# Optimization experiments

Measured on AMD Instinct MI355X. Metric: run time of the kernel, lower is better.

The kernel has to match this reference:

```python
import jax, jax.numpy as jnp
import numpy as np


def setup_inputs() -> dict:
    key = jax.random.key(0)
    k1, k2, k3 = jax.random.split(key, 3)
    B, Q, K, D = 4, 2048, 2048, 1024
    query = jax.random.normal(k1, (B, Q, D), dtype=jnp.float32)
    value = jax.random.normal(k2, (B, K, D), dtype=jnp.float32)
    attention_mask = jax.random.randint(k3, (B, Q, K), 0, 2, dtype=jnp.int32)
    return {"query": query, "value": value, "attention_mask": attention_mask}


def reference(query, value, attention_mask):
    # key defaults to value in the original module
    D = query.shape[-1]
    # scores[b,q,k] = sum_d (query[b,q,d] + key[b,k,d])
    #              = rowsum(query)[b,q] + rowsum(key)[b,k]  (separable outer-sum,
    # avoids the (B,Q,K,D) intermediate the torch code materializes)
    q_sum = query.sum(-1)                    # (B, Q)
    k_sum = value.sum(-1)                    # (B, K)  (key == value)
    scores = q_sum[:, :, None] + k_sum[:, None, :]   # (B, Q, K)
    scores = scores / jnp.sqrt(jnp.asarray(D, scores.dtype))  # use_scale=True
    mask_value = -1e9
    scores = scores + (1.0 - attention_mask.astype(scores.dtype)) * mask_value
    attention_weights = jax.nn.softmax(scores, axis=-1)       # (B, Q, K)
    context_vector = jnp.einsum('bqk,bkd->bqd', attention_weights, value)
    return (context_vector, attention_weights)
```

## Files before the change

kernel.cpp:

```cpp
#include <hip/hip_runtime.h>
#include <stdint.h>

#define BB 4
#define QQ 2048
#define KK 2048
#define DD 1024

__device__ inline unsigned short f2bf(float f) {
    unsigned int u = __float_as_uint(f);
    unsigned int r = (u + 0x7fffu + ((u >> 16) & 1u)) >> 16;
    return (unsigned short)r;
}

typedef short bf16x8 __attribute__((ext_vector_type(8)));
typedef float f32x4  __attribute__((ext_vector_type(4)));

__device__ inline void async16(const void* g, void* l) {
    __builtin_amdgcn_global_load_lds(
        (const __attribute__((address_space(1))) unsigned int*)g,
        (__attribute__((address_space(3))) unsigned int*)l,
        16, 0, 0);
}

__global__ __launch_bounds__(256) void transpose_sum(const float* __restrict__ V,
                                                     unsigned short* __restrict__ Vt,
                                                     float* __restrict__ s) {
    int bid = blockIdx.x;
    int b  = bid >> 9;
    int r  = bid & 511;
    int kt = r >> 4;
    int dt = r & 15;
    int k0 = kt * 64, d0 = dt * 64;
    __shared__ float tile[64 * 65];
    int t = threadIdx.x;
    for (int i = 0; i < 4; i++) {
        int idx = i * 256 + t;
        int row = idx >> 4;
        int c4  = idx & 15;
        float4 v = *(const float4*)(V + (size_t)(b * KK + k0 + row) * DD + d0 + c4 * 4);
        float* p = &tile[row * 65 + c4 * 4];
        p[0] = v.x; p[1] = v.y; p[2] = v.z; p[3] = v.w;
        float ps = (v.x + v.y) + (v.z + v.w);
        ps += __shfl_xor(ps, 8, 16);
        ps += __shfl_xor(ps, 4, 16);
        ps += __shfl_xor(ps, 2, 16);
        ps += __shfl_xor(ps, 1, 16);
        if (c4 == 0) atomicAdd(s + (size_t)b * KK + k0 + row, ps);
    }
    __syncthreads();
    for (int i = 0; i < 4; i++) {
        int idx = i * 256 + t;
        int dr = idx >> 4;
        int kc = idx & 15;
        ushort4 o;
        o.x = f2bf(tile[(kc * 4 + 0) * 65 + dr]);
        o.y = f2bf(tile[(kc * 4 + 1) * 65 + dr]);
        o.z = f2bf(tile[(kc * 4 + 2) * 65 + dr]);
        o.w = f2bf(tile[(kc * 4 + 3) * 65 + dr]);
        *(ushort4*)(Vt + (size_t)(b * DD + d0 + dr) * KK + k0 + kc * 4) = o;
    }
}

__global__ __launch_bounds__(256) void weights_k(const int* __restrict__ mask,
                                                 const float* __restrict__ s,
                                                 float* __restrict__ wout,
                                                 unsigned short* __restrict__ wb16) {
    int wave = threadIdx.x >> 6, lane = threadIdx.x & 63;
    int row = blockIdx.x * 4 + wave;
    int b = row >> 11;
    const int4*   mp = (const int4*)(mask + (size_t)row * KK);
    const float4* ep = (const float4*)(s + (size_t)b * KK);
    float4 w[8];
    float ss = 0.f;
    for (int j = 0; j < 8; j++) {
        int4   m  = mp[lane + j * 64];
        float4 sv = ep[lane + j * 64];
        float4 ev;
        ev.x = __expf(sv.x * 0.03125f);
        ev.y = __expf(sv.y * 0.03125f);
        ev.z = __expf(sv.z * 0.03125f);
        ev.w = __expf(sv.w * 0.03125f);
        w[j].x = m.x ? ev.x : 0.f;
        w[j].y = m.y ? ev.y : 0.f;
        w[j].z = m.z ? ev.z : 0.f;
        w[j].w = m.w ? ev.w : 0.f;
        ss += (w[j].x + w[j].y) + (w[j].z + w[j].w);
    }
    for (int off = 32; off; off >>= 1) ss += __shfl_xor(ss, off, 64);
    float rS = 1.f / ss;
    float4*  wp = (float4*)(wout + (size_t)row * KK);
    ushort4* bp = (ushort4*)(wb16 + (size_t)row * KK);
    for (int j = 0; j < 8; j++) {
        float4 v = w[j];
        v.x *= rS; v.y *= rS; v.z *= rS; v.w *= rS;
        wp[lane + j * 64] = v;
        ushort4 pk;
        pk.x = f2bf(v.x); pk.y = f2bf(v.y); pk.z = f2bf(v.z); pk.w = f2bf(v.w);
        bp[lane + j * 64] = pk;
    }
}

__global__ __launch_bounds__(256) void gemm_ctx(const unsigned short* __restrict__ Wb,
                                                const unsigned short* __restrict__ Vt,
                                                float* __restrict__ ctx) {
    int bid = blockIdx.x;
    int dt = bid >> 6;
    int b  = (bid >> 4) & 3;
    int qt = bid & 15;
    int q0 = qt * 128, n0 = dt * 128;
    __shared__ unsigned short As[2][128 * 64];
    __shared__ unsigned short Bs[2][128 * 64];
    int tid = threadIdx.x, wave = tid >> 6, lane = tid & 63;
    int quad = lane >> 4, lm = lane & 15;
    int wm = wave >> 1, wn = wave & 1;

    int srow   = lane >> 3;
    int schunk = (lane & 7) ^ srow;
    const unsigned short* Ag = Wb + (size_t)(b * QQ + q0 + wave * 8 + srow) * KK + schunk * 8;
    const unsigned short* Bg = Vt + (size_t)(b * DD + n0 + wave * 8 + srow) * KK + schunk * 8;
    unsigned short* lA0 = &As[0][(wave * 8) * 64];
    unsigned short* lA1 = &As[1][(wave * 8) * 64];
    unsigned short* lB0 = &Bs[0][(wave * 8) * 64];
    unsigned short* lB1 = &Bs[1][(wave * 8) * 64];

    int m7 = lm & 7;
    int xa0 = lm * 64 + ((0 + quad) ^ m7) * 8;
    int xa1 = lm * 64 + ((4 + quad) ^ m7) * 8;

    f32x4 acc[4][4];
    for (int i = 0; i < 4; i++)
        for (int j = 0; j < 4; j++) acc[i][j] = 0.f;

#define STAGE(dA, dB, kpos) do {                                           \
        for (int c = 0; c < 4; c++) {                                      \
            async16(Ag + (size_t)(c * 32) * KK + (kpos), (dA) + c * 32 * 64); \
            async16(Bg + (size_t)(c * 32) * KK + (kpos), (dB) + c * 32 * 64); \
        }                                                                  \
    } while (0)

#define COMPUTE(Ab, Bb) do {                                               \
        bf16x8 a[4][2], bv[4][2];                                          \
        for (int i = 0; i < 4; i++) {                                      \
            a[i][0]  = *(const bf16x8*)&(Ab)[(wm * 64 + i * 16) * 64 + xa0]; \
            a[i][1]  = *(const bf16x8*)&(Ab)[(wm * 64 + i * 16) * 64 + xa1]; \
            bv[i][0] = *(const bf16x8*)&(Bb)[(wn * 64 + i * 16) * 64 + xa0]; \
            bv[i][1] = *(const bf16x8*)&(Bb)[(wn * 64 + i * 16) * 64 + xa1]; \
        }                                                                  \
        for (int h = 0; h < 2; h++)                                        \
            for (int i = 0; i < 4; i++)                                    \
                for (int j = 0; j < 4; j++)                                \
                    acc[i][j] = __builtin_amdgcn_mfma_f32_16x16x32_bf16(   \
                        a[i][h], bv[j][h], acc[i][j], 0, 0, 0);            \
    } while (0)

#define DRAIN_BARRIER() do {                                               \
        __builtin_amdgcn_sched_barrier(0);                                 \
        asm volatile("s_waitcnt vmcnt(0) lgkmcnt(0)" ::: "memory");        \
        __builtin_amdgcn_s_barrier();                                      \
    } while (0)

    STAGE(lA0, lB0, 0);
    DRAIN_BARRIER();

    for (int t = 0; t < 32; t += 2) {
        STAGE(lA1, lB1, (t + 1) * 64);
        COMPUTE(&As[0][0], &Bs[0][0]);
        DRAIN_BARRIER();
        if (t + 2 < 32) STAGE(lA0, lB0, (t + 2) * 64);
        COMPUTE(&As[1][0], &Bs[1][0]);
        if (t + 2 < 32) DRAIN_BARRIER();
    }

#undef STAGE
#undef COMPUTE
#undef DRAIN_BARRIER

    for (int i = 0; i < 4; i++) {
        int rowb = q0 + wm * 64 + i * 16 + quad * 4;
        for (int j = 0; j < 4; j++) {
            int col = n0 + wn * 64 + j * 16 + lm;
            for (int rr = 0; rr < 4; rr++)
                ctx[(size_t)(b * QQ + rowb + rr) * DD + col] = acc[i][j][rr];
        }
    }
}

extern "C" void kernel_launch(void* const* d_in, const int* in_sizes, int n_in,
                              void* d_out, int out_size, void* d_ws, size_t ws_size,
                              hipStream_t stream) {
    const float* value = (const float*)d_in[1];
    const int*   mask  = (const int*)d_in[2];
    float* out = (float*)d_out;

    unsigned short* Vt = (unsigned short*)d_ws;
    unsigned short* Wb = Vt + (size_t)BB * DD * KK;
    float* s = (float*)(Wb + (size_t)BB * QQ * KK);

    float* ctx  = out;
    float* wout = out + (size_t)BB * QQ * DD;

    hipMemsetAsync(s, 0, (size_t)BB * KK * sizeof(float), stream);
    transpose_sum<<<BB * 512, 256, 0, stream>>>(value, Vt, s);
    weights_k<<<(BB * QQ) / 4, 256, 0, stream>>>(mask, s, wout, Wb);
    gemm_ctx<<<BB * 128, 256, 0, stream>>>(Wb, Vt, ctx);
}
```

Measured before the change: 242.1 us.

## Triple-buffer B tiles with two-deep prefetch and partial vmcnt waits in ctx GEMM

The context GEMM now keeps three LDS buffers for the V^T operand and two for the weight operand. It prefetches B two K-steps ahead and A one step ahead. Each iteration waits with vmcnt(4) instead of draining every outstanding load, so the newest B loads stay in flight across the barrier. The main loop is also fully unrolled. The cost is more LDS per block (80KB instead of 64KB) and larger code, which could limit occupancy or instruction cache behaviour.

```diff
diff --git a/kernel.cpp b/kernel.cpp
--- a/kernel.cpp
+++ b/kernel.cpp
@@ -109,7 +109,7 @@
     int qt = bid & 15;
     int q0 = qt * 128, n0 = dt * 128;
     __shared__ unsigned short As[2][128 * 64];
-    __shared__ unsigned short Bs[2][128 * 64];
+    __shared__ unsigned short Bs[3][128 * 64];
     int tid = threadIdx.x, wave = tid >> 6, lane = tid & 63;
     int quad = lane >> 4, lm = lane & 15;
     int wm = wave >> 1, wn = wave & 1;
@@ -118,10 +118,6 @@
     int schunk = (lane & 7) ^ srow;
     const unsigned short* Ag = Wb + (size_t)(b * QQ + q0 + wave * 8 + srow) * KK + schunk * 8;
     const unsigned short* Bg = Vt + (size_t)(b * DD + n0 + wave * 8 + srow) * KK + schunk * 8;
-    unsigned short* lA0 = &As[0][(wave * 8) * 64];
-    unsigned short* lA1 = &As[1][(wave * 8) * 64];
-    unsigned short* lB0 = &Bs[0][(wave * 8) * 64];
-    unsigned short* lB1 = &Bs[1][(wave * 8) * 64];
 
     int m7 = lm & 7;
     int xa0 = lm * 64 + ((0 + quad) ^ m7) * 8;
@@ -131,49 +127,60 @@
     for (int i = 0; i < 4; i++)
         for (int j = 0; j < 4; j++) acc[i][j] = 0.f;
 
-#define STAGE(dA, dB, kpos) do {                                           \
-        for (int c = 0; c < 4; c++) {                                      \
-            async16(Ag + (size_t)(c * 32) * KK + (kpos), (dA) + c * 32 * 64); \
-            async16(Bg + (size_t)(c * 32) * KK + (kpos), (dB) + c * 32 * 64); \
-        }                                                                  \
+#define STAGE_A(buf, kpos) do {                                               \
+        unsigned short* d = &As[buf][(wave * 8) * 64];                        \
+        for (int c = 0; c < 4; c++)                                           \
+            async16(Ag + (size_t)(c * 32) * KK + (kpos), d + c * 32 * 64);    \
     } while (0)
 
-#define COMPUTE(Ab, Bb) do {                                               \
-        bf16x8 a[4][2], bv[4][2];                                          \
-        for (int i = 0; i < 4; i++) {                                      \
-            a[i][0]  = *(const bf16x8*)&(Ab)[(wm * 64 + i * 16) * 64 + xa0]; \
-            a[i][1]  = *(const bf16x8*)&(Ab)[(wm * 64 + i * 16) * 64 + xa1]; \
-            bv[i][0] = *(const bf16x8*)&(Bb)[(wn * 64 + i * 16) * 64 + xa0]; \
-            bv[i][1] = *(const bf16x8*)&(Bb)[(wn * 64 + i * 16) * 64 + xa1]; \
-        }                                                                  \
-        for (int h = 0; h < 2; h++)                                        \
-            for (int i = 0; i < 4; i++)                                    \
-                for (int j = 0; j < 4; j++)                                \
-                    acc[i][j] = __builtin_amdgcn_mfma_f32_16x16x32_bf16(   \
-                        a[i][h], bv[j][h], acc[i][j], 0, 0, 0);            \
+#define STAGE_B(buf, kpos) do {                                               \
+        unsigned short* d = &Bs[buf][(wave * 8) * 64];                        \
+        for (int c = 0; c < 4; c++)                                           \
+            async16(Bg + (size_t)(c * 32) * KK + (kpos), d + c * 32 * 64);    \
     } while (0)
 
-#define DRAIN_BARRIER() do {                                               \
-        __builtin_amdgcn_sched_barrier(0);                                 \
-        asm volatile("s_waitcnt vmcnt(0) lgkmcnt(0)" ::: "memory");        \
-        __builtin_amdgcn_s_barrier();                                      \
+#define COMPUTE(ab, bb) do {                                                  \
+        bf16x8 a[4][2], bv[4][2];                                             \
+        for (int i = 0; i < 4; i++) {                                         \
+            a[i][0]  = *(const bf16x8*)&As[ab][(wm * 64 + i * 16) * 64 + xa0]; \
+            a[i][1]  = *(const bf16x8*)&As[ab][(wm * 64 + i * 16) * 64 + xa1]; \
+            bv[i][0] = *(const bf16x8*)&Bs[bb][(wn * 64 + i * 16) * 64 + xa0]; \
+            bv[i][1] = *(const bf16x8*)&Bs[bb][(wn * 64 + i * 16) * 64 + xa1]; \
+        }                                                                     \
+        for (int h = 0; h < 2; h++)                                           \
+            for (int i = 0; i < 4; i++)                                       \
+                for (int j = 0; j < 4; j++)                                   \
+                    acc[i][j] = __builtin_amdgcn_mfma_f32_16x16x32_bf16(      \
+                        a[i][h], bv[j][h], acc[i][j], 0, 0, 0);               \
     } while (0)
 
-    STAGE(lA0, lB0, 0);
-    DRAIN_BARRIER();
-
-    for (int t = 0; t < 32; t += 2) {
-        STAGE(lA1, lB1, (t + 1) * 64);
-        COMPUTE(&As[0][0], &Bs[0][0]);
-        DRAIN_BARRIER();
-        if (t + 2 < 32) STAGE(lA0, lB0, (t + 2) * 64);
-        COMPUTE(&As[1][0], &Bs[1][0]);
-        if (t + 2 < 32) DRAIN_BARRIER();
-    }
-
-#undef STAGE
+    STAGE_A(0, 0);
+    STAGE_B(0, 0);
+    STAGE_B(1, 64);
+    __builtin_amdgcn_sched_barrier(0);
+    asm volatile("s_waitcnt vmcnt(4)" ::: "memory");
+    __builtin_amdgcn_s_barrier();
+
+#pragma unroll
+    for (int t = 0; t < 32; ++t) {
+        if (t + 1 < 32) STAGE_A((t + 1) & 1, (t + 1) * 64);
+        if (t + 2 < 32) STAGE_B((t + 2) % 3, (t + 2) * 64);
+        COMPUTE(t & 1, t % 3);
+        if (t + 1 < 32) {
+            __builtin_amdgcn_sched_barrier(0);
+            if (t + 2 < 32) {
+                asm volatile("s_waitcnt vmcnt(4)" ::: "memory");
+            } else {
+                asm volatile("s_waitcnt vmcnt(0)" ::: "memory");
+            }
+            __builtin_amdgcn_sched_barrier(0);
+            __builtin_amdgcn_s_barrier();
+        }
+    }
+
+#undef STAGE_A
+#undef STAGE_B
 #undef COMPUTE
-#undef DRAIN_BARRIER
 
     for (int i = 0; i < 4; i++) {
         int rowb = q0 + wm * 64 + i * 16 + quad * 4;
```

Result: no change. 240.1 us (-0.8%).
